# Performance work log

Measured on AMD Instinct MI355X. Metric: run time of the kernel, lower is better.

Reference implementation:

```python
import jax, jax.numpy as jnp
import numpy as np

H = 4  # attention heads
NEG = -1e9

def _ln(x, g, b):
    m = jnp.mean(x, -1, keepdims=True)
    v = jnp.var(x, -1, keepdims=True)
    return g * (x - m) * jax.lax.rsqrt(v + 1e-5) + b

def setup_inputs() -> dict:
    key = jax.random.key(0)
    ks = jax.random.split(key, 32)
    N, E, G, T = 4096, 128, 10, 10
    f32 = jnp.float32
    def w(k, shape, fan):
        return (jax.random.normal(k, shape, f32) / np.sqrt(fan)).astype(f32)
    inp = {
        'lora_states': jax.random.normal(ks[0], (N, 256), f32),
        'temperaments': jax.random.uniform(ks[1], (N, T), f32),
        'adjacency': jax.random.randint(ks[2], (N, N), 0, 2, jnp.int32),
        'memory_bank': jax.random.normal(ks[3], (G, E), f32) * 0.1,
        # lora_state_encoder: Linear(256,512) -> LN -> ReLU -> Linear(512,E) -> LN
        'enc_W1': w(ks[4], (256, 512), 256), 'enc_b1': jnp.zeros((512,), f32),
        'enc_g1': jnp.ones((512,), f32), 'enc_be1': jnp.zeros((512,), f32),
        'enc_W2': w(ks[5], (512, E), 512), 'enc_b2': jnp.zeros((E,), f32),
        'enc_g2': jnp.ones((E,), f32), 'enc_be2': jnp.zeros((E,), f32),
        # TemperamentEncoder: Linear(10,E) + tanh
        'temp_W': w(ks[6], (T, E), T), 'temp_b': jnp.zeros((E,), f32),
        # SocialAttentionLayer (adjacency-masked MHA)
        'Wq': w(ks[7], (E, E), E), 'Wk': w(ks[8], (E, E), E),
        'Wv': w(ks[9], (E, E), E), 'Wo': w(ks[10], (E, E), E),
        # PersonalityModulatedAttention scalar gate over [my_temp; ctx_j]
        'gate_wa': w(ks[11], (E,), E), 'gate_wb': w(ks[12], (E,), E),
        'gate_b': jnp.zeros((), f32),
        # lora_state_decoder: Linear(E,512) -> LN -> ReLU -> Linear(512,256)
        'dec_W1': w(ks[13], (E, 512), E), 'dec_b1': jnp.zeros((512,), f32),
        'dec_g1': jnp.ones((512,), f32), 'dec_be1': jnp.zeros((512,), f32),
        'dec_W2': w(ks[14], (512, 256), 512), 'dec_b2': jnp.zeros((256,), f32),
    }
    return inp

def reference(lora_states, temperaments, adjacency, memory_bank,
              enc_W1, enc_b1, enc_g1, enc_be1, enc_W2, enc_b2, enc_g2, enc_be2,
              temp_W, temp_b, Wq, Wk, Wv, Wo, gate_wa, gate_wb, gate_b,
              dec_W1, dec_b1, dec_g1, dec_be1, dec_W2, dec_b2):
    N = lora_states.shape[0]
    E = Wq.shape[0]
    dh = E // H
    # --- encode LoRA states ---
    h = jax.nn.relu(_ln(lora_states @ enc_W1 + enc_b1, enc_g1, enc_be1))
    emb = _ln(h @ enc_W2 + enc_b2, enc_g2, enc_be2)                  # [N,E]
    # --- temperament embeddings ---
    temp_emb = jnp.tanh(temperaments @ temp_W + temp_b)              # [N,E]
    # --- adjacency-masked multi-head social attention ---
    q = (emb @ Wq).reshape(N, H, dh).transpose(1, 0, 2)              # [H,N,dh]
    k = (emb @ Wk).reshape(N, H, dh).transpose(1, 0, 2)
    v = (emb @ Wv).reshape(N, H, dh).transpose(1, 0, 2)
    scores = jnp.einsum('hnd,hmd->hnm', q, k) / np.sqrt(dh)          # [H,N,N]
    adj = adjacency > 0
    eye = jnp.eye(N, dtype=bool)
    attn = jax.nn.softmax(jnp.where((adj | eye)[None], scores, NEG), axis=-1)
    ctx = jnp.einsum('hnm,hmd->hnd', attn, v).transpose(1, 0, 2).reshape(N, E) @ Wo  # [N,E]
    # --- personality-gated neighbor aggregation (scalar gate per (i,j)) ---
    ti = temp_emb @ gate_wa                                          # [N]
    cj = ctx @ gate_wb                                               # [N]
    gate = jax.nn.sigmoid(ti[:, None] + cj[None, :] + gate_b)        # [N,N]
    nmask = (adj & ~eye).astype(emb.dtype)                           # exclude self
    cnt = nmask.sum(-1)                                              # [N]
    combined = (nmask * gate) @ ctx / jnp.maximum(cnt, 1.0)[:, None] # mean of gated neighbor infos
    updated = emb + 0.2 * jnp.where(cnt[:, None] > 0, combined, 0.0)
    # --- generational memory retrieval: 0.9*emb + 0.1*ancestral ---
    mscore = updated @ memory_bank.T / np.sqrt(E)                    # [N,G]
    ancestral = jax.nn.softmax(mscore, axis=-1) @ memory_bank        # [N,E]
    updated = 0.9 * updated + 0.1 * ancestral
    # --- decode back to LoRA state vectors ---
    d = jax.nn.relu(_ln(updated @ dec_W1 + dec_b1, dec_g1, dec_be1))
    return d @ dec_W2 + dec_b2                                       # [N,256]
```

## Files before the change

kernel.cpp:

```cpp
#include <hip/hip_runtime.h>
#include <math.h>

#define N 4096
#define NHEAD 4
#define SPLIT_ATT 8
#define SPLIT_G 8

__global__ __launch_bounds__(256) void k_bm(const int* __restrict__ adj,
    unsigned int* __restrict__ bmw) {
  const int lane = threadIdx.x & 63;
  const int wid = threadIdx.x >> 6;
  const long total = (long)N * N / 64;
  long g = (long)blockIdx.x * 4 + wid;
  const long stride = (long)gridDim.x * 4;
  for (; g < total; g += stride) {
    int e = adj[g * 64 + lane];
    unsigned long long mask = __ballot(e != 0);
    if (lane == 0)  bmw[g * 2]     = (unsigned int)(mask & 0xFFFFFFFFull);
    if (lane == 32) bmw[g * 2 + 1] = (unsigned int)(mask >> 32);
  }
}

__global__ __launch_bounds__(512) void k_enc1(const float* __restrict__ X,
    const float* __restrict__ W, const float* __restrict__ b,
    const float* __restrict__ g, const float* __restrict__ be,
    float* __restrict__ out) {
  __shared__ float xs[8][256];
  __shared__ float hs[8][512];
  const int t = threadIdx.x;
  const int row0 = blockIdx.x * 8;
  {
    const float4* src = reinterpret_cast<const float4*>(X + row0 * 256);
    float4* dst = reinterpret_cast<float4*>(&xs[0][0]);
    dst[t] = src[t];
  }
  __syncthreads();
  float acc[8] = {0.f,0.f,0.f,0.f,0.f,0.f,0.f,0.f};
  for (int k = 0; k < 256; ++k) {
    float w = W[k * 512 + t];
#pragma unroll
    for (int r = 0; r < 8; ++r) acc[r] = fmaf(xs[r][k], w, acc[r]);
  }
  const float bb = b[t];
#pragma unroll
  for (int r = 0; r < 8; ++r) hs[r][t] = acc[r] + bb;
  __syncthreads();
  const int wv = t >> 6, lane = t & 63;
  float v0[8];
  float s1 = 0.f, s2 = 0.f;
#pragma unroll
  for (int kk = 0; kk < 8; ++kk) {
    float x = hs[wv][lane + 64 * kk];
    v0[kk] = x; s1 += x; s2 += x * x;
  }
#pragma unroll
  for (int off = 1; off < 64; off <<= 1) { s1 += __shfl_xor(s1, off); s2 += __shfl_xor(s2, off); }
  const float mean = s1 * (1.f / 512.f);
  const float var = s2 * (1.f / 512.f) - mean * mean;
  const float rstd = rsqrtf(var + 1e-5f);
#pragma unroll
  for (int kk = 0; kk < 8; ++kk) {
    int c = lane + 64 * kk;
    float y = g[c] * (v0[kk] - mean) * rstd + be[c];
    out[(row0 + wv) * 512 + c] = fmaxf(y, 0.f);
  }
}

__global__ __launch_bounds__(128) void k_enc2(const float* __restrict__ X,
    const float* __restrict__ W, const float* __restrict__ b,
    const float* __restrict__ g, const float* __restrict__ be,
    float* __restrict__ out) {
  __shared__ float xs[8][512];
  __shared__ float hs[8][128];
  const int t = threadIdx.x;
  const int row0 = blockIdx.x * 8;
  {
    const float4* src = reinterpret_cast<const float4*>(X + row0 * 512);
    float4* dst = reinterpret_cast<float4*>(&xs[0][0]);
    for (int idx = t; idx < 1024; idx += 128) dst[idx] = src[idx];
  }
  __syncthreads();
  float acc[8] = {0.f,0.f,0.f,0.f,0.f,0.f,0.f,0.f};
  for (int k = 0; k < 512; ++k) {
    float w = W[k * 128 + t];
#pragma unroll
    for (int r = 0; r < 8; ++r) acc[r] = fmaf(xs[r][k], w, acc[r]);
  }
  const float bb = b[t];
#pragma unroll
  for (int r = 0; r < 8; ++r) hs[r][t] = acc[r] + bb;
  __syncthreads();
  const int wv = t >> 6, lane = t & 63;
  for (int rr = 0; rr < 4; ++rr) {
    int row = wv * 4 + rr;
    float a0 = hs[row][lane], a1 = hs[row][lane + 64];
    float s1 = a0 + a1, s2 = a0 * a0 + a1 * a1;
#pragma unroll
    for (int off = 1; off < 64; off <<= 1) { s1 += __shfl_xor(s1, off); s2 += __shfl_xor(s2, off); }
    float mean = s1 * (1.f / 128.f);
    float rstd = rsqrtf(s2 * (1.f / 128.f) - mean * mean + 1e-5f);
    out[(row0 + row) * 128 + lane]      = g[lane] * (a0 - mean) * rstd + be[lane];
    out[(row0 + row) * 128 + lane + 64] = g[lane + 64] * (a1 - mean) * rstd + be[lane + 64];
  }
}

__global__ __launch_bounds__(512) void k_qkv(const float* __restrict__ emb,
    const float* __restrict__ Wq, const float* __restrict__ Wk, const float* __restrict__ Wv,
    float* __restrict__ q, float* __restrict__ k, float* __restrict__ v) {
  __shared__ float xs[16][128];
  const int t = threadIdx.x;
  const int col = t & 127;
  const int grp = t >> 7;
  const int row0 = blockIdx.x * 16;
  {
    const float4* src = reinterpret_cast<const float4*>(emb + row0 * 128);
    float4* dst = reinterpret_cast<float4*>(&xs[0][0]);
    dst[t] = src[t];
  }
  __syncthreads();
  float aq[4] = {0.f,0.f,0.f,0.f};
  float ak[4] = {0.f,0.f,0.f,0.f};
  float av[4] = {0.f,0.f,0.f,0.f};
  for (int kk = 0; kk < 128; ++kk) {
    float wq = Wq[kk * 128 + col], wk = Wk[kk * 128 + col], wv = Wv[kk * 128 + col];
#pragma unroll
    for (int r = 0; r < 4; ++r) {
      float x = xs[grp * 4 + r][kk];
      aq[r] = fmaf(x, wq, aq[r]);
      ak[r] = fmaf(x, wk, ak[r]);
      av[r] = fmaf(x, wv, av[r]);
    }
  }
#pragma unroll
  for (int r = 0; r < 4; ++r) {
    const int row = row0 + grp * 4 + r;
    q[row * 128 + col] = aq[r];
    k[row * 128 + col] = ak[r];
    v[row * 128 + col] = av[r];
  }
}

__global__ __launch_bounds__(256) void k_ti(const float* __restrict__ temps,
    const float* __restrict__ tW, const float* __restrict__ tb,
    const float* __restrict__ wa, float* __restrict__ ti_out) {
  __shared__ float tws[1280];
  __shared__ float tbs[128], was[128];
  const int t = threadIdx.x;
  for (int idx = t; idx < 1280; idx += 256) tws[idx] = tW[idx];
  if (t < 128) { tbs[t] = tb[t]; was[t] = wa[t]; }
  __syncthreads();
  const int qi = t & 3;
  const int li = t >> 2;
  const int i = blockIdx.x * 64 + li;
  float tp[10];
#pragma unroll
  for (int c = 0; c < 10; ++c) tp[c] = temps[i * 10 + c];
  float acc = 0.f;
  const int e0 = qi * 32;
  for (int e = e0; e < e0 + 32; ++e) {
    float s = tbs[e];
#pragma unroll
    for (int c = 0; c < 10; ++c) s = fmaf(tp[c], tws[c * 128 + e], s);
    float th = 1.f - 2.f * __fdividef(1.f, __expf(2.f * s) + 1.f);
    acc = fmaf(th, was[e], acc);
  }
  acc += __shfl_xor(acc, 1);
  acc += __shfl_xor(acc, 2);
  if (qi == 0) ti_out[i] = acc;
}

__global__ __launch_bounds__(256, 2) void k_attn(const float* __restrict__ q,
    const float* __restrict__ kk, const float* __restrict__ vv,
    const unsigned int* __restrict__ bmw,
    float* __restrict__ pacc, float* __restrict__ pml) {
  __shared__ float Kt[64][128];
  __shared__ float Vt[64][128];
  const int t = threadIdx.x;
  const int itile = blockIdx.x / SPLIT_ATT;
  const int split = blockIdx.x % SPLIT_ATT;
  const int h = t >> 6;
  const int row = t & 63;
  const int i = itile * 64 + row;
  const int dbase = h * 32;
  float4 q4[8];
  {
    const float4* qp = reinterpret_cast<const float4*>(q + (size_t)i * 128 + dbase);
#pragma unroll
    for (int u = 0; u < 8; ++u) q4[u] = qp[u];
  }
  float m = -1e30f, l = 0.f;
  float4 a[8];
#pragma unroll
  for (int u = 0; u < 8; ++u) a[u] = make_float4(0.f, 0.f, 0.f, 0.f);
  const int j0beg = split * (N / SPLIT_ATT);
  const int j0end = j0beg + (N / SPLIT_ATT);
  for (int j0 = j0beg; j0 < j0end; j0 += 64) {
    __syncthreads();
    {
      const float4* ks = reinterpret_cast<const float4*>(kk + (size_t)j0 * 128);
      const float4* vs = reinterpret_cast<const float4*>(vv + (size_t)j0 * 128);
      float4* kd = reinterpret_cast<float4*>(&Kt[0][0]);
      float4* vd = reinterpret_cast<float4*>(&Vt[0][0]);
#pragma unroll
      for (int u = 0; u < 8; ++u) { kd[t + 256 * u] = ks[t + 256 * u]; vd[t + 256 * u] = vs[t + 256 * u]; }
    }
    const uint2 mw = *reinterpret_cast<const uint2*>(bmw + (size_t)i * 128 + (j0 >> 5));
    const int eyeoff = i - j0;
    __syncthreads();
    for (int sub = 0; sub < 8; ++sub) {
      const int jb = sub * 8;
      unsigned mbits = ((sub < 4 ? mw.x : mw.y) >> ((sub & 3) * 8)) & 0xFFu;
      if (((unsigned)(eyeoff - jb)) < 8u) mbits |= (1u << (eyeoff - jb));
      float sarr[8];
#pragma unroll
      for (int u = 0; u < 8; ++u) {
        const float4* kp = reinterpret_cast<const float4*>(&Kt[jb + u][dbase]);
        float4 kf[8];
#pragma unroll
        for (int w = 0; w < 8; ++w) kf[w] = kp[w];
        float s0 = 0.f, s1 = 0.f, s2 = 0.f, s3 = 0.f;
#pragma unroll
        for (int w = 0; w < 8; ++w) {
          s0 = fmaf(q4[w].x, kf[w].x, s0);
          s1 = fmaf(q4[w].y, kf[w].y, s1);
          s2 = fmaf(q4[w].z, kf[w].z, s2);
          s3 = fmaf(q4[w].w, kf[w].w, s3);
        }
        sarr[u] = fmaf((s0 + s1) + (s2 + s3), 0.17677669529663687f,
                       ((mbits >> u) & 1u) ? 0.f : -1e9f);
      }
      float smax = fmaxf(fmaxf(fmaxf(sarr[0], sarr[1]), fmaxf(sarr[2], sarr[3])),
                         fmaxf(fmaxf(sarr[4], sarr[5]), fmaxf(sarr[6], sarr[7])));
      float mnew = fmaxf(m, smax);
      float r = __expf(m - mnew);
      m = mnew;
      l *= r;
#pragma unroll
      for (int u = 0; u < 8; ++u) {
        a[u].x *= r; a[u].y *= r; a[u].z *= r; a[u].w *= r;
      }
#pragma unroll
      for (int u = 0; u < 8; ++u) {
        float p = __expf(sarr[u] - m);
        l += p;
        const float4* vp = reinterpret_cast<const float4*>(&Vt[jb + u][dbase]);
#pragma unroll
        for (int w = 0; w < 8; ++w) {
          float4 vf = vp[w];
          a[w].x = fmaf(p, vf.x, a[w].x);
          a[w].y = fmaf(p, vf.y, a[w].y);
          a[w].z = fmaf(p, vf.z, a[w].z);
          a[w].w = fmaf(p, vf.w, a[w].w);
        }
      }
    }
  }
  {
    float4* pa4 = reinterpret_cast<float4*>(pacc + ((size_t)split * N + i) * 128 + dbase);
#pragma unroll
    for (int u = 0; u < 8; ++u) pa4[u] = a[u];
  }
  {
    float2* p2 = reinterpret_cast<float2*>(pml + (((size_t)split * N + i) * NHEAD + h) * 2);
    *p2 = make_float2(m, l);
  }
}

__global__ __launch_bounds__(256) void k_attn_comb(const float* __restrict__ pacc,
    const float* __restrict__ pml, float* __restrict__ attnout) {
  const int gid = blockIdx.x * 256 + threadIdx.x;
  const int i = gid >> 7, e = gid & 127, h = e >> 5;
  float ms[SPLIT_ATT], ls[SPLIT_ATT];
  float M = -1e30f;
#pragma unroll
  for (int s = 0; s < SPLIT_ATT; ++s) {
    size_t idx = (((size_t)s * N + i) * NHEAD + h) * 2;
    ms[s] = pml[idx]; ls[s] = pml[idx + 1];
    M = fmaxf(M, ms[s]);
  }
  float L = 0.f, o = 0.f;
#pragma unroll
  for (int s = 0; s < SPLIT_ATT; ++s) {
    float w = expf(ms[s] - M);
    L = fmaf(ls[s], w, L);
    o = fmaf(pacc[((size_t)(s * N + i)) * 128 + e], w, o);
  }
  attnout[gid] = o / L;
}

__global__ __launch_bounds__(128) void k_ctx(const float* __restrict__ att,
    const float* __restrict__ Wo, const float* __restrict__ wb,
    float* __restrict__ ctx, float* __restrict__ cj) {
  __shared__ float xs[8][128];
  __shared__ float hs[8][128];
  const int t = threadIdx.x;
  const int row0 = blockIdx.x * 8;
  {
    const float4* src = reinterpret_cast<const float4*>(att + row0 * 128);
    float4* dst = reinterpret_cast<float4*>(&xs[0][0]);
    for (int idx = t; idx < 256; idx += 128) dst[idx] = src[idx];
  }
  __syncthreads();
  float acc[8] = {0.f,0.f,0.f,0.f,0.f,0.f,0.f,0.f};
  for (int k = 0; k < 128; ++k) {
    float w = Wo[k * 128 + t];
#pragma unroll
    for (int r = 0; r < 8; ++r) acc[r] = fmaf(xs[r][k], w, acc[r]);
  }
  const float wbt = wb[t];
#pragma unroll
  for (int r = 0; r < 8; ++r) {
    ctx[(row0 + r) * 128 + t] = acc[r];
    hs[r][t] = acc[r] * wbt;
  }
  __syncthreads();
  const int wv = t >> 6, lane = t & 63;
  for (int rr = 0; rr < 4; ++rr) {
    int row = wv * 4 + rr;
    float s1 = hs[row][lane] + hs[row][lane + 64];
#pragma unroll
    for (int off = 1; off < 64; off <<= 1) s1 += __shfl_xor(s1, off);
    if (lane == 0) cj[row0 + row] = s1;
  }
}

__global__ __launch_bounds__(256) void k_gate(const float* __restrict__ ctx,
    const float* __restrict__ cj, const float* __restrict__ ti,
    const unsigned int* __restrict__ bmw, const float* __restrict__ gbp,
    float* __restrict__ pacc, float* __restrict__ pcnt) {
  __shared__ float cs[64][128];
  __shared__ float gtsT[64][65];
  __shared__ float tis[64];
  __shared__ float cntrow[64];
  __shared__ float pcsum[256];
  const int t = threadIdx.x;
  const int itile = blockIdx.x >> 3;
  const int split = blockIdx.x & 7;
  const int ig = t >> 4;
  const int eg = t & 15;
  const int i0 = itile * 64;
  const float gb = gbp[0];
  if (t < 64) { tis[t] = ti[i0 + t]; cntrow[t] = 0.f; }
  float acc[4][8];
#pragma unroll
  for (int r = 0; r < 4; ++r)
#pragma unroll
    for (int c = 0; c < 8; ++c) acc[r][c] = 0.f;
  const int j0beg = split * (N / SPLIT_G);
  const int j0end = j0beg + (N / SPLIT_G);
  for (int j0 = j0beg; j0 < j0end; j0 += 64) {
    __syncthreads();
    {
      const float4* src = reinterpret_cast<const float4*>(ctx + (size_t)j0 * 128);
      float4* dst = reinterpret_cast<float4*>(&cs[0][0]);
#pragma unroll
      for (int u = 0; u < 8; ++u) dst[t + 256 * u] = src[t + 256 * u];
    }
    {
      const int ii = t >> 2;
      const int qd = t & 3;
      const int jb = qd * 16;
      const int gi = i0 + ii;
      const float tii = tis[ii];
      const unsigned word = bmw[(size_t)gi * 128 + (j0 >> 5) + (qd >> 1)];
      const unsigned mb16 = (word >> ((qd & 1) * 16)) & 0xFFFFu;
      float cnt_loc = 0.f;
      const float4* cjp = reinterpret_cast<const float4*>(cj + j0 + jb);
      float4 cv[4];
#pragma unroll
      for (int u = 0; u < 4; ++u) cv[u] = cjp[u];
      const float cva[16] = {cv[0].x,cv[0].y,cv[0].z,cv[0].w, cv[1].x,cv[1].y,cv[1].z,cv[1].w,
                             cv[2].x,cv[2].y,cv[2].z,cv[2].w, cv[3].x,cv[3].y,cv[3].z,cv[3].w};
#pragma unroll
      for (int w = 0; w < 16; ++w) {
        const int gj = j0 + jb + w;
        const bool live = ((mb16 >> w) & 1u) && (gj != gi);
        float gval = 0.f;
        if (live) {
          gval = __fdividef(1.f, 1.f + __expf(-(tii + cva[w] + gb)));
          cnt_loc += 1.f;
        }
        gtsT[jb + w][ii] = gval;
      }
      pcsum[t] = cnt_loc;
    }
    __syncthreads();
    if (t < 64) {
      cntrow[t] += pcsum[t * 4] + pcsum[t * 4 + 1] + pcsum[t * 4 + 2] + pcsum[t * 4 + 3];
    }
    const int ib = ig * 4;
    const int eb = eg * 8;
    for (int jj = 0; jj < 64; ++jj) {
      const float a0 = gtsT[jj][ib + 0];
      const float a1 = gtsT[jj][ib + 1];
      const float a2 = gtsT[jj][ib + 2];
      const float a3 = gtsT[jj][ib + 3];
      const float4 b0 = *reinterpret_cast<const float4*>(&cs[jj][eb]);
      const float4 b1 = *reinterpret_cast<const float4*>(&cs[jj][eb + 4]);
      const float bv[8] = {b0.x, b0.y, b0.z, b0.w, b1.x, b1.y, b1.z, b1.w};
#pragma unroll
      for (int c = 0; c < 8; ++c) {
        acc[0][c] = fmaf(a0, bv[c], acc[0][c]);
        acc[1][c] = fmaf(a1, bv[c], acc[1][c]);
        acc[2][c] = fmaf(a2, bv[c], acc[2][c]);
        acc[3][c] = fmaf(a3, bv[c], acc[3][c]);
      }
    }
  }
#pragma unroll
  for (int r = 0; r < 4; ++r) {
    float* pa = pacc + ((size_t)split * N + i0 + ig * 4 + r) * 128 + eg * 8;
    float4 o0; o0.x = acc[r][0]; o0.y = acc[r][1]; o0.z = acc[r][2]; o0.w = acc[r][3];
    float4 o1; o1.x = acc[r][4]; o1.y = acc[r][5]; o1.z = acc[r][6]; o1.w = acc[r][7];
    reinterpret_cast<float4*>(pa)[0] = o0;
    reinterpret_cast<float4*>(pa)[1] = o1;
  }
  if (t < 64) pcnt[(size_t)split * N + i0 + t] = cntrow[t];
}

__global__ __launch_bounds__(256) void k_gcomb(const float* __restrict__ GA,
    const float* __restrict__ GC, const float* __restrict__ emb,
    const float* __restrict__ mb, float* __restrict__ upd) {
  __shared__ float mbs[10][128];
  __shared__ float us[2][128];
  const int t = threadIdx.x;
  for (int idx = t; idx < 1280; idx += 256) mbs[idx / 128][idx & 127] = mb[idx];
  const int rs = t >> 7, e = t & 127;
  const int i = blockIdx.x * 2 + rs;
  float a = 0.f;
#pragma unroll
  for (int s = 0; s < SPLIT_G; ++s) a += GA[((size_t)(s * N + i)) * 128 + e];
  float c = 0.f;
#pragma unroll
  for (int s = 0; s < SPLIT_G; ++s) c += GC[s * N + i];
  float comb = a / fmaxf(c, 1.f);
  float u = emb[(size_t)i * 128 + e] + 0.2f * ((c > 0.f) ? comb : 0.f);
  us[rs][e] = u;
  __syncthreads();
  const int wv = t >> 6, lane = t & 63;
  if (wv < 2) {
    const int i2 = blockIdx.x * 2 + wv;
    float u0 = us[wv][lane], u1 = us[wv][lane + 64];
    float sc[10];
#pragma unroll
    for (int g = 0; g < 10; ++g) {
      float p = u0 * mbs[g][lane] + u1 * mbs[g][lane + 64];
#pragma unroll
      for (int off = 1; off < 64; off <<= 1) p += __shfl_xor(p, off);
      sc[g] = p * 0.08838834764831845f;
    }
    float mx = sc[0];
#pragma unroll
    for (int g = 1; g < 10; ++g) mx = fmaxf(mx, sc[g]);
    float sum = 0.f;
#pragma unroll
    for (int g = 0; g < 10; ++g) { sc[g] = expf(sc[g] - mx); sum += sc[g]; }
    float inv = 1.f / sum;
    float anc0 = 0.f, anc1 = 0.f;
#pragma unroll
    for (int g = 0; g < 10; ++g) {
      float pg = sc[g] * inv;
      anc0 = fmaf(pg, mbs[g][lane], anc0);
      anc1 = fmaf(pg, mbs[g][lane + 64], anc1);
    }
    upd[(size_t)i2 * 128 + lane]      = 0.9f * u0 + 0.1f * anc0;
    upd[(size_t)i2 * 128 + lane + 64] = 0.9f * u1 + 0.1f * anc1;
  }
}

__global__ __launch_bounds__(512) void k_dec1(const float* __restrict__ X,
    const float* __restrict__ W, const float* __restrict__ b,
    const float* __restrict__ g, const float* __restrict__ be,
    float* __restrict__ out) {
  __shared__ float xs[8][128];
  __shared__ float hs[8][512];
  const int t = threadIdx.x;
  const int row0 = blockIdx.x * 8;
  if (t < 256) {
    const float4* src = reinterpret_cast<const float4*>(X + row0 * 128);
    float4* dst = reinterpret_cast<float4*>(&xs[0][0]);
    dst[t] = src[t];
  }
  __syncthreads();
  float acc[8] = {0.f,0.f,0.f,0.f,0.f,0.f,0.f,0.f};
  for (int k = 0; k < 128; ++k) {
    float w = W[k * 512 + t];
#pragma unroll
    for (int r = 0; r < 8; ++r) acc[r] = fmaf(xs[r][k], w, acc[r]);
  }
  const float bb = b[t];
#pragma unroll
  for (int r = 0; r < 8; ++r) hs[r][t] = acc[r] + bb;
  __syncthreads();
  const int wv = t >> 6, lane = t & 63;
  float v0[8];
  float s1 = 0.f, s2 = 0.f;
#pragma unroll
  for (int kk = 0; kk < 8; ++kk) {
    float x = hs[wv][lane + 64 * kk];
    v0[kk] = x; s1 += x; s2 += x * x;
  }
#pragma unroll
  for (int off = 1; off < 64; off <<= 1) { s1 += __shfl_xor(s1, off); s2 += __shfl_xor(s2, off); }
  const float mean = s1 * (1.f / 512.f);
  const float var = s2 * (1.f / 512.f) - mean * mean;
  const float rstd = rsqrtf(var + 1e-5f);
#pragma unroll
  for (int kk = 0; kk < 8; ++kk) {
    int c = lane + 64 * kk;
    float y = g[c] * (v0[kk] - mean) * rstd + be[c];
    out[(row0 + wv) * 512 + c] = fmaxf(y, 0.f);
  }
}

__global__ __launch_bounds__(256) void k_dec2(const float* __restrict__ X,
    const float* __restrict__ W, const float* __restrict__ b, float* __restrict__ out) {
  __shared__ float xs[8][512];
  const int t = threadIdx.x;
  const int row0 = blockIdx.x * 8;
  {
    const float4* src = reinterpret_cast<const float4*>(X + row0 * 512);
    float4* dst = reinterpret_cast<float4*>(&xs[0][0]);
    for (int idx = t; idx < 1024; idx += 256) dst[idx] = src[idx];
  }
  __syncthreads();
  float acc[8] = {0.f,0.f,0.f,0.f,0.f,0.f,0.f,0.f};
  for (int k = 0; k < 512; ++k) {
    float w = W[k * 256 + t];
#pragma unroll
    for (int r = 0; r < 8; ++r) acc[r] = fmaf(xs[r][k], w, acc[r]);
  }
  const float bb = b[t];
#pragma unroll
  for (int r = 0; r < 8; ++r) out[(row0 + r) * 256 + t] = acc[r] + bb;
}

extern "C" void kernel_launch(void* const* d_in, const int* in_sizes, int n_in,
                              void* d_out, int out_size, void* d_ws, size_t ws_size,
                              hipStream_t stream) {
  const float* lora   = (const float*)d_in[0];
  const float* temps  = (const float*)d_in[1];
  const int*   adj    = (const int*)d_in[2];
  const float* mb     = (const float*)d_in[3];
  const float* enc_W1 = (const float*)d_in[4];
  const float* enc_b1 = (const float*)d_in[5];
  const float* enc_g1 = (const float*)d_in[6];
  const float* enc_be1= (const float*)d_in[7];
  const float* enc_W2 = (const float*)d_in[8];
  const float* enc_b2 = (const float*)d_in[9];
  const float* enc_g2 = (const float*)d_in[10];
  const float* enc_be2= (const float*)d_in[11];
  const float* temp_W = (const float*)d_in[12];
  const float* temp_b = (const float*)d_in[13];
  const float* Wq     = (const float*)d_in[14];
  const float* Wk     = (const float*)d_in[15];
  const float* Wv     = (const float*)d_in[16];
  const float* Wo     = (const float*)d_in[17];
  const float* g_wa   = (const float*)d_in[18];
  const float* g_wb   = (const float*)d_in[19];
  const float* g_b    = (const float*)d_in[20];
  const float* dec_W1 = (const float*)d_in[21];
  const float* dec_b1 = (const float*)d_in[22];
  const float* dec_g1 = (const float*)d_in[23];
  const float* dec_be1= (const float*)d_in[24];
  const float* dec_W2 = (const float*)d_in[25];
  const float* dec_b2 = (const float*)d_in[26];

  float* ws = (float*)d_ws;
  float* H1  = ws;
  float* EMB = H1 + (size_t)N * 512;
  float* Q   = EMB + (size_t)N * 128;
  float* K   = Q + (size_t)N * 128;
  float* V   = K + (size_t)N * 128;
  float* ATT = V + (size_t)N * 128;
  float* CTX = ATT + (size_t)N * 128;
  float* TI  = CTX + (size_t)N * 128;
  float* CJ  = TI + N;
  float* PA  = CJ + N;
  float* PML = PA + (size_t)8 * N * 128;
  unsigned int* BMW = (unsigned int*)(PML + (size_t)8 * N * NHEAD * 2);
  float* UPD = ATT;
  float* GA  = PA;
  float* GC  = PML;
  float* DEC = H1;

  k_bm<<<512, 256, 0, stream>>>(adj, BMW);
  k_enc1<<<N / 8, 512, 0, stream>>>(lora, enc_W1, enc_b1, enc_g1, enc_be1, H1);
  k_enc2<<<N / 8, 128, 0, stream>>>(H1, enc_W2, enc_b2, enc_g2, enc_be2, EMB);
  k_ti<<<N / 64, 256, 0, stream>>>(temps, temp_W, temp_b, g_wa, TI);
  k_qkv<<<N / 16, 512, 0, stream>>>(EMB, Wq, Wk, Wv, Q, K, V);
  k_attn<<<(N / 64) * SPLIT_ATT, 256, 0, stream>>>(Q, K, V, BMW, PA, PML);
  k_attn_comb<<<(N * 128) / 256, 256, 0, stream>>>(PA, PML, ATT);
  k_ctx<<<N / 8, 128, 0, stream>>>(ATT, Wo, g_wb, CTX, CJ);
  k_gate<<<(N / 64) * SPLIT_G, 256, 0, stream>>>(CTX, CJ, TI, BMW, g_b, GA, GC);
  k_gcomb<<<N / 2, 256, 0, stream>>>(GA, GC, EMB, mb, UPD);
  k_dec1<<<N / 8, 512, 0, stream>>>(UPD, dec_W1, dec_b1, dec_g1, dec_be1, DEC);
  k_dec2<<<N / 8, 256, 0, stream>>>(DEC, dec_W2, dec_b2, (float*)d_out);
}
```

Baseline: 716.7 us.

## Retune attention split and tiles, vectorize LDS reads in dense GEMM kernels

```diff
diff --git a/kernel.cpp b/kernel.cpp
--- a/kernel.cpp
+++ b/kernel.cpp
@@ -3,7 +3,7 @@
 
 #define N 4096
 #define NHEAD 4
-#define SPLIT_ATT 8
+#define SPLIT_ATT 16
 #define SPLIT_G 8
 
 __global__ __launch_bounds__(256) void k_bm(const int* __restrict__ adj,
@@ -21,7 +21,7 @@
   }
 }
 
-__global__ __launch_bounds__(512) void k_enc1(const float* __restrict__ X,
+__global__ __launch_bounds__(256) void k_enc1(const float* __restrict__ X,
     const float* __restrict__ W, const float* __restrict__ b,
     const float* __restrict__ g, const float* __restrict__ be,
     float* __restrict__ out) {
@@ -32,41 +32,57 @@
   {
     const float4* src = reinterpret_cast<const float4*>(X + row0 * 256);
     float4* dst = reinterpret_cast<float4*>(&xs[0][0]);
-    dst[t] = src[t];
-  }
-  __syncthreads();
-  float acc[8] = {0.f,0.f,0.f,0.f,0.f,0.f,0.f,0.f};
-  for (int k = 0; k < 256; ++k) {
-    float w = W[k * 512 + t];
-#pragma unroll
-    for (int r = 0; r < 8; ++r) acc[r] = fmaf(xs[r][k], w, acc[r]);
-  }
-  const float bb = b[t];
-#pragma unroll
-  for (int r = 0; r < 8; ++r) hs[r][t] = acc[r] + bb;
+    dst[t] = src[t]; dst[t + 256] = src[t + 256];
+  }
+  __syncthreads();
+  float acc0[8], acc1[8];
+#pragma unroll
+  for (int r = 0; r < 8; ++r) { acc0[r] = 0.f; acc1[r] = 0.f; }
+  for (int k4 = 0; k4 < 64; ++k4) {
+    const int k = k4 * 4;
+    const float w00 = W[(k + 0) * 512 + t];
+    const float w01 = W[(k + 1) * 512 + t];
+    const float w02 = W[(k + 2) * 512 + t];
+    const float w03 = W[(k + 3) * 512 + t];
+    const float w10 = W[(k + 0) * 512 + t + 256];
+    const float w11 = W[(k + 1) * 512 + t + 256];
+    const float w12 = W[(k + 2) * 512 + t + 256];
+    const float w13 = W[(k + 3) * 512 + t + 256];
+#pragma unroll
+    for (int r = 0; r < 8; ++r) {
+      const float4 xv = *reinterpret_cast<const float4*>(&xs[r][k]);
+      acc0[r] = fmaf(xv.x, w00, fmaf(xv.y, w01, fmaf(xv.z, w02, fmaf(xv.w, w03, acc0[r]))));
+      acc1[r] = fmaf(xv.x, w10, fmaf(xv.y, w11, fmaf(xv.z, w12, fmaf(xv.w, w13, acc1[r]))));
+    }
+  }
+  const float b0 = b[t], b1 = b[t + 256];
+#pragma unroll
+  for (int r = 0; r < 8; ++r) { hs[r][t] = acc0[r] + b0; hs[r][t + 256] = acc1[r] + b1; }
   __syncthreads();
   const int wv = t >> 6, lane = t & 63;
-  float v0[8];
-  float s1 = 0.f, s2 = 0.f;
-#pragma unroll
-  for (int kk = 0; kk < 8; ++kk) {
-    float x = hs[wv][lane + 64 * kk];
-    v0[kk] = x; s1 += x; s2 += x * x;
-  }
-#pragma unroll
-  for (int off = 1; off < 64; off <<= 1) { s1 += __shfl_xor(s1, off); s2 += __shfl_xor(s2, off); }
-  const float mean = s1 * (1.f / 512.f);
-  const float var = s2 * (1.f / 512.f) - mean * mean;
-  const float rstd = rsqrtf(var + 1e-5f);
-#pragma unroll
-  for (int kk = 0; kk < 8; ++kk) {
-    int c = lane + 64 * kk;
-    float y = g[c] * (v0[kk] - mean) * rstd + be[c];
-    out[(row0 + wv) * 512 + c] = fmaxf(y, 0.f);
-  }
-}
-
-__global__ __launch_bounds__(128) void k_enc2(const float* __restrict__ X,
+  for (int rr = 0; rr < 2; ++rr) {
+    const int row = wv * 2 + rr;
+    float v0[8];
+    float s1 = 0.f, s2 = 0.f;
+#pragma unroll
+    for (int kk = 0; kk < 8; ++kk) {
+      float x = hs[row][lane + 64 * kk];
+      v0[kk] = x; s1 += x; s2 += x * x;
+    }
+#pragma unroll
+    for (int off = 1; off < 64; off <<= 1) { s1 += __shfl_xor(s1, off); s2 += __shfl_xor(s2, off); }
+    const float mean = s1 * (1.f / 512.f);
+    const float rstd = rsqrtf(s2 * (1.f / 512.f) - mean * mean + 1e-5f);
+#pragma unroll
+    for (int kk = 0; kk < 8; ++kk) {
+      int c = lane + 64 * kk;
+      float y = g[c] * (v0[kk] - mean) * rstd + be[c];
+      out[(row0 + row) * 512 + c] = fmaxf(y, 0.f);
+    }
+  }
+}
+
+__global__ __launch_bounds__(256) void k_enc2(const float* __restrict__ X,
     const float* __restrict__ W, const float* __restrict__ b,
     const float* __restrict__ g, const float* __restrict__ be,
     float* __restrict__ out) {
@@ -77,22 +93,32 @@
   {
     const float4* src = reinterpret_cast<const float4*>(X + row0 * 512);
     float4* dst = reinterpret_cast<float4*>(&xs[0][0]);
-    for (int idx = t; idx < 1024; idx += 128) dst[idx] = src[idx];
-  }
-  __syncthreads();
-  float acc[8] = {0.f,0.f,0.f,0.f,0.f,0.f,0.f,0.f};
-  for (int k = 0; k < 512; ++k) {
-    float w = W[k * 128 + t];
-#pragma unroll
-    for (int r = 0; r < 8; ++r) acc[r] = fmaf(xs[r][k], w, acc[r]);
-  }
-  const float bb = b[t];
-#pragma unroll
-  for (int r = 0; r < 8; ++r) hs[r][t] = acc[r] + bb;
+#pragma unroll
+    for (int u = 0; u < 4; ++u) dst[t + 256 * u] = src[t + 256 * u];
+  }
+  __syncthreads();
+  const int col = t & 127;
+  const int rg = t >> 7;
+  float acc[4] = {0.f,0.f,0.f,0.f};
+  for (int k4 = 0; k4 < 128; ++k4) {
+    const int k = k4 * 4;
+    const float w0 = W[(k + 0) * 128 + col];
+    const float w1 = W[(k + 1) * 128 + col];
+    const float w2 = W[(k + 2) * 128 + col];
+    const float w3 = W[(k + 3) * 128 + col];
+#pragma unroll
+    for (int r = 0; r < 4; ++r) {
+      const float4 xv = *reinterpret_cast<const float4*>(&xs[rg * 4 + r][k]);
+      acc[r] = fmaf(xv.x, w0, fmaf(xv.y, w1, fmaf(xv.z, w2, fmaf(xv.w, w3, acc[r]))));
+    }
+  }
+  const float bb = b[col];
+#pragma unroll
+  for (int r = 0; r < 4; ++r) hs[rg * 4 + r][col] = acc[r] + bb;
   __syncthreads();
   const int wv = t >> 6, lane = t & 63;
-  for (int rr = 0; rr < 4; ++rr) {
-    int row = wv * 4 + rr;
+  for (int rr = 0; rr < 2; ++rr) {
+    const int row = wv * 2 + rr;
     float a0 = hs[row][lane], a1 = hs[row][lane + 64];
     float s1 = a0 + a1, s2 = a0 * a0 + a1 * a1;
 #pragma unroll
@@ -121,14 +147,17 @@
   float aq[4] = {0.f,0.f,0.f,0.f};
   float ak[4] = {0.f,0.f,0.f,0.f};
   float av[4] = {0.f,0.f,0.f,0.f};
-  for (int kk = 0; kk < 128; ++kk) {
-    float wq = Wq[kk * 128 + col], wk = Wk[kk * 128 + col], wv = Wv[kk * 128 + col];
+  for (int k4 = 0; k4 < 32; ++k4) {
+    const int kk = k4 * 4;
+    float wq0 = Wq[(kk+0)*128+col], wq1 = Wq[(kk+1)*128+col], wq2 = Wq[(kk+2)*128+col], wq3 = Wq[(kk+3)*128+col];
+    float wk0 = Wk[(kk+0)*128+col], wk1 = Wk[(kk+1)*128+col], wk2 = Wk[(kk+2)*128+col], wk3 = Wk[(kk+3)*128+col];
+    float wv0 = Wv[(kk+0)*128+col], wv1 = Wv[(kk+1)*128+col], wv2 = Wv[(kk+2)*128+col], wv3 = Wv[(kk+3)*128+col];
 #pragma unroll
     for (int r = 0; r < 4; ++r) {
-      float x = xs[grp * 4 + r][kk];
-      aq[r] = fmaf(x, wq, aq[r]);
-      ak[r] = fmaf(x, wk, ak[r]);
-      av[r] = fmaf(x, wv, av[r]);
+      const float4 xv = *reinterpret_cast<const float4*>(&xs[grp * 4 + r][kk]);
+      aq[r] = fmaf(xv.x, wq0, fmaf(xv.y, wq1, fmaf(xv.z, wq2, fmaf(xv.w, wq3, aq[r]))));
+      ak[r] = fmaf(xv.x, wk0, fmaf(xv.y, wk1, fmaf(xv.z, wk2, fmaf(xv.w, wk3, ak[r]))));
+      av[r] = fmaf(xv.x, wv0, fmaf(xv.y, wv1, fmaf(xv.z, wv2, fmaf(xv.w, wv3, av[r]))));
     }
   }
 #pragma unroll
@@ -169,12 +198,12 @@
   if (qi == 0) ti_out[i] = acc;
 }
 
-__global__ __launch_bounds__(256, 2) void k_attn(const float* __restrict__ q,
+__global__ __launch_bounds__(256, 4) void k_attn(const float* __restrict__ q,
     const float* __restrict__ kk, const float* __restrict__ vv,
     const unsigned int* __restrict__ bmw,
     float* __restrict__ pacc, float* __restrict__ pml) {
-  __shared__ float Kt[64][128];
-  __shared__ float Vt[64][128];
+  __shared__ float Kt[32][128];
+  __shared__ float Vt[32][128];
   const int t = threadIdx.x;
   const int itile = blockIdx.x / SPLIT_ATT;
   const int split = blockIdx.x % SPLIT_ATT;
@@ -192,9 +221,10 @@
   float4 a[8];
 #pragma unroll
   for (int u = 0; u < 8; ++u) a[u] = make_float4(0.f, 0.f, 0.f, 0.f);
-  const int j0beg = split * (N / SPLIT_ATT);
-  const int j0end = j0beg + (N / SPLIT_ATT);
-  for (int j0 = j0beg; j0 < j0end; j0 += 64) {
+  const int jrange = N / SPLIT_ATT;
+  const int j0beg = split * jrange;
+  const int j0end = j0beg + jrange;
+  for (int j0 = j0beg; j0 < j0end; j0 += 32) {
     __syncthreads();
     {
       const float4* ks = reinterpret_cast<const float4*>(kk + (size_t)j0 * 128);
@@ -202,14 +232,14 @@
       float4* kd = reinterpret_cast<float4*>(&Kt[0][0]);
       float4* vd = reinterpret_cast<float4*>(&Vt[0][0]);
 #pragma unroll
-      for (int u = 0; u < 8; ++u) { kd[t + 256 * u] = ks[t + 256 * u]; vd[t + 256 * u] = vs[t + 256 * u]; }
-    }
-    const uint2 mw = *reinterpret_cast<const uint2*>(bmw + (size_t)i * 128 + (j0 >> 5));
+      for (int u = 0; u < 4; ++u) { kd[t + 256 * u] = ks[t + 256 * u]; vd[t + 256 * u] = vs[t + 256 * u]; }
+    }
+    const unsigned mword = bmw[(size_t)i * 128 + (j0 >> 5)];
     const int eyeoff = i - j0;
     __syncthreads();
-    for (int sub = 0; sub < 8; ++sub) {
+    for (int sub = 0; sub < 4; ++sub) {
       const int jb = sub * 8;
-      unsigned mbits = ((sub < 4 ? mw.x : mw.y) >> ((sub & 3) * 8)) & 0xFFu;
+      unsigned mbits = (mword >> jb) & 0xFFu;
       if (((unsigned)(eyeoff - jb)) < 8u) mbits |= (1u << (eyeoff - jb));
       float sarr[8];
 #pragma unroll
@@ -217,27 +247,29 @@
         const float4* kp = reinterpret_cast<const float4*>(&Kt[jb + u][dbase]);
         float4 kf[8];
 #pragma unroll
-        for (int w = 0; w < 8; ++w) kf[w] = kp[w];
+        for (int x = 0; x < 8; ++x) kf[x] = kp[x];
         float s0 = 0.f, s1 = 0.f, s2 = 0.f, s3 = 0.f;
 #pragma unroll
-        for (int w = 0; w < 8; ++w) {
-          s0 = fmaf(q4[w].x, kf[w].x, s0);
-          s1 = fmaf(q4[w].y, kf[w].y, s1);
-          s2 = fmaf(q4[w].z, kf[w].z, s2);
-          s3 = fmaf(q4[w].w, kf[w].w, s3);
+        for (int x = 0; x < 8; ++x) {
+          s0 = fmaf(q4[x].x, kf[x].x, s0);
+          s1 = fmaf(q4[x].y, kf[x].y, s1);
+          s2 = fmaf(q4[x].z, kf[x].z, s2);
+          s3 = fmaf(q4[x].w, kf[x].w, s3);
         }
         sarr[u] = fmaf((s0 + s1) + (s2 + s3), 0.17677669529663687f,
                        ((mbits >> u) & 1u) ? 0.f : -1e9f);
       }
       float smax = fmaxf(fmaxf(fmaxf(sarr[0], sarr[1]), fmaxf(sarr[2], sarr[3])),
                          fmaxf(fmaxf(sarr[4], sarr[5]), fmaxf(sarr[6], sarr[7])));
-      float mnew = fmaxf(m, smax);
-      float r = __expf(m - mnew);
-      m = mnew;
-      l *= r;
-#pragma unroll
-      for (int u = 0; u < 8; ++u) {
-        a[u].x *= r; a[u].y *= r; a[u].z *= r; a[u].w *= r;
+      if (__any(smax > m)) {
+        float mnew = fmaxf(m, smax);
+        float r = __expf(m - mnew);
+        m = mnew;
+        l *= r;
+#pragma unroll
+        for (int u = 0; u < 8; ++u) {
+          a[u].x *= r; a[u].y *= r; a[u].z *= r; a[u].w *= r;
+        }
       }
 #pragma unroll
       for (int u = 0; u < 8; ++u) {
@@ -245,12 +277,12 @@
         l += p;
         const float4* vp = reinterpret_cast<const float4*>(&Vt[jb + u][dbase]);
 #pragma unroll
-        for (int w = 0; w < 8; ++w) {
-          float4 vf = vp[w];
-          a[w].x = fmaf(p, vf.x, a[w].x);
-          a[w].y = fmaf(p, vf.y, a[w].y);
-          a[w].z = fmaf(p, vf.z, a[w].z);
-          a[w].w = fmaf(p, vf.w, a[w].w);
+        for (int x = 0; x < 8; ++x) {
+          float4 vf = vp[x];
+          a[x].x = fmaf(p, vf.x, a[x].x);
+          a[x].y = fmaf(p, vf.y, a[x].y);
+          a[x].z = fmaf(p, vf.z, a[x].z);
+          a[x].w = fmaf(p, vf.w, a[x].w);
         }
       }
     }
@@ -288,36 +320,45 @@
   attnout[gid] = o / L;
 }
 
-__global__ __launch_bounds__(128) void k_ctx(const float* __restrict__ att,
+__global__ __launch_bounds__(512) void k_ctx(const float* __restrict__ att,
     const float* __restrict__ Wo, const float* __restrict__ wb,
     float* __restrict__ ctx, float* __restrict__ cj) {
-  __shared__ float xs[8][128];
-  __shared__ float hs[8][128];
-  const int t = threadIdx.x;
-  const int row0 = blockIdx.x * 8;
+  __shared__ float xs[16][128];
+  __shared__ float hs[16][128];
+  const int t = threadIdx.x;
+  const int row0 = blockIdx.x * 16;
   {
     const float4* src = reinterpret_cast<const float4*>(att + row0 * 128);
     float4* dst = reinterpret_cast<float4*>(&xs[0][0]);
-    for (int idx = t; idx < 256; idx += 128) dst[idx] = src[idx];
-  }
-  __syncthreads();
-  float acc[8] = {0.f,0.f,0.f,0.f,0.f,0.f,0.f,0.f};
-  for (int k = 0; k < 128; ++k) {
-    float w = Wo[k * 128 + t];
-#pragma unroll
-    for (int r = 0; r < 8; ++r) acc[r] = fmaf(xs[r][k], w, acc[r]);
-  }
-  const float wbt = wb[t];
-#pragma unroll
-  for (int r = 0; r < 8; ++r) {
-    ctx[(row0 + r) * 128 + t] = acc[r];
-    hs[r][t] = acc[r] * wbt;
+    dst[t] = src[t];
+  }
+  __syncthreads();
+  const int col = t & 127;
+  const int grp = t >> 7;
+  float acc[4] = {0.f,0.f,0.f,0.f};
+  for (int k4 = 0; k4 < 32; ++k4) {
+    const int k = k4 * 4;
+    const float w0 = Wo[(k + 0) * 128 + col];
+    const float w1 = Wo[(k + 1) * 128 + col];
+    const float w2 = Wo[(k + 2) * 128 + col];
+    const float w3 = Wo[(k + 3) * 128 + col];
+#pragma unroll
+    for (int r = 0; r < 4; ++r) {
+      const float4 xv = *reinterpret_cast<const float4*>(&xs[grp * 4 + r][k]);
+      acc[r] = fmaf(xv.x, w0, fmaf(xv.y, w1, fmaf(xv.z, w2, fmaf(xv.w, w3, acc[r]))));
+    }
+  }
+#pragma unroll
+  for (int r = 0; r < 4; ++r) {
+    ctx[(row0 + grp * 4 + r) * 128 + col] = acc[r];
+    hs[grp * 4 + r][col] = acc[r];
   }
   __syncthreads();
   const int wv = t >> 6, lane = t & 63;
-  for (int rr = 0; rr < 4; ++rr) {
-    int row = wv * 4 + rr;
-    float s1 = hs[row][lane] + hs[row][lane + 64];
+  const float wb0 = wb[lane], wb1 = wb[lane + 64];
+  for (int rr = 0; rr < 2; ++rr) {
+    const int row = wv * 2 + rr;
+    float s1 = hs[row][lane] * wb0 + hs[row][lane + 64] * wb1;
 #pragma unroll
     for (int off = 1; off < 64; off <<= 1) s1 += __shfl_xor(s1, off);
     if (lane == 0) cj[row0 + row] = s1;
@@ -468,7 +509,7 @@
   }
 }
 
-__global__ __launch_bounds__(512) void k_dec1(const float* __restrict__ X,
+__global__ __launch_bounds__(256) void k_dec1(const float* __restrict__ X,
     const float* __restrict__ W, const float* __restrict__ b,
     const float* __restrict__ g, const float* __restrict__ be,
     float* __restrict__ out) {
@@ -476,40 +517,56 @@
   __shared__ float hs[8][512];
   const int t = threadIdx.x;
   const int row0 = blockIdx.x * 8;
-  if (t < 256) {
+  {
     const float4* src = reinterpret_cast<const float4*>(X + row0 * 128);
     float4* dst = reinterpret_cast<float4*>(&xs[0][0]);
     dst[t] = src[t];
   }
   __syncthreads();
-  float acc[8] = {0.f,0.f,0.f,0.f,0.f,0.f,0.f,0.f};
-  for (int k = 0; k < 128; ++k) {
-    float w = W[k * 512 + t];
-#pragma unroll
-    for (int r = 0; r < 8; ++r) acc[r] = fmaf(xs[r][k], w, acc[r]);
-  }
-  const float bb = b[t];
-#pragma unroll
-  for (int r = 0; r < 8; ++r) hs[r][t] = acc[r] + bb;
+  float acc0[8], acc1[8];
+#pragma unroll
+  for (int r = 0; r < 8; ++r) { acc0[r] = 0.f; acc1[r] = 0.f; }
+  for (int k4 = 0; k4 < 32; ++k4) {
+    const int k = k4 * 4;
+    const float w00 = W[(k + 0) * 512 + t];
+    const float w01 = W[(k + 1) * 512 + t];
+    const float w02 = W[(k + 2) * 512 + t];
+    const float w03 = W[(k + 3) * 512 + t];
+    const float w10 = W[(k + 0) * 512 + t + 256];
+    const float w11 = W[(k + 1) * 512 + t + 256];
+    const float w12 = W[(k + 2) * 512 + t + 256];
+    const float w13 = W[(k + 3) * 512 + t + 256];
+#pragma unroll
+    for (int r = 0; r < 8; ++r) {
+      const float4 xv = *reinterpret_cast<const float4*>(&xs[r][k]);
+      acc0[r] = fmaf(xv.x, w00, fmaf(xv.y, w01, fmaf(xv.z, w02, fmaf(xv.w, w03, acc0[r]))));
+      acc1[r] = fmaf(xv.x, w10, fmaf(xv.y, w11, fmaf(xv.z, w12, fmaf(xv.w, w13, acc1[r]))));
+    }
+  }
+  const float b0 = b[t], b1 = b[t + 256];
+#pragma unroll
+  for (int r = 0; r < 8; ++r) { hs[r][t] = acc0[r] + b0; hs[r][t + 256] = acc1[r] + b1; }
   __syncthreads();
   const int wv = t >> 6, lane = t & 63;
-  float v0[8];
-  float s1 = 0.f, s2 = 0.f;
-#pragma unroll
-  for (int kk = 0; kk < 8; ++kk) {
-    float x = hs[wv][lane + 64 * kk];
-    v0[kk] = x; s1 += x; s2 += x * x;
-  }
-#pragma unroll
-  for (int off = 1; off < 64; off <<= 1) { s1 += __shfl_xor(s1, off); s2 += __shfl_xor(s2, off); }
-  const float mean = s1 * (1.f / 512.f);
-  const float var = s2 * (1.f / 512.f) - mean * mean;
-  const float rstd = rsqrtf(var + 1e-5f);
-#pragma unroll
-  for (int kk = 0; kk < 8; ++kk) {
-    int c = lane + 64 * kk;
-    float y = g[c] * (v0[kk] - mean) * rstd + be[c];
-    out[(row0 + wv) * 512 + c] = fmaxf(y, 0.f);
+  for (int rr = 0; rr < 2; ++rr) {
+    const int row = wv * 2 + rr;
+    float v0[8];
+    float s1 = 0.f, s2 = 0.f;
+#pragma unroll
+    for (int kk = 0; kk < 8; ++kk) {
+      float x = hs[row][lane + 64 * kk];
+      v0[kk] = x; s1 += x; s2 += x * x;
+    }
+#pragma unroll
+    for (int off = 1; off < 64; off <<= 1) { s1 += __shfl_xor(s1, off); s2 += __shfl_xor(s2, off); }
+    const float mean = s1 * (1.f / 512.f);
+    const float rstd = rsqrtf(s2 * (1.f / 512.f) - mean * mean + 1e-5f);
+#pragma unroll
+    for (int kk = 0; kk < 8; ++kk) {
+      int c = lane + 64 * kk;
+      float y = g[c] * (v0[kk] - mean) * rstd + be[c];
+      out[(row0 + row) * 512 + c] = fmaxf(y, 0.f);
+    }
   }
 }
 
@@ -521,14 +578,24 @@
   {
     const float4* src = reinterpret_cast<const float4*>(X + row0 * 512);
     float4* dst = reinterpret_cast<float4*>(&xs[0][0]);
-    for (int idx = t; idx < 1024; idx += 256) dst[idx] = src[idx];
-  }
-  __syncthreads();
-  float acc[8] = {0.f,0.f,0.f,0.f,0.f,0.f,0.f,0.f};
-  for (int k = 0; k < 512; ++k) {
-    float w = W[k * 256 + t];
-#pragma unroll
-    for (int r = 0; r < 8; ++r) acc[r] = fmaf(xs[r][k], w, acc[r]);
+#pragma unroll
+    for (int u = 0; u < 4; ++u) dst[t + 256 * u] = src[t + 256 * u];
+  }
+  __syncthreads();
+  float acc[8];
+#pragma unroll
+  for (int r = 0; r < 8; ++r) acc[r] = 0.f;
+  for (int k4 = 0; k4 < 128; ++k4) {
+    const int k = k4 * 4;
+    const float w0 = W[(k + 0) * 256 + t];
+    const float w1 = W[(k + 1) * 256 + t];
+    const float w2 = W[(k + 2) * 256 + t];
+    const float w3 = W[(k + 3) * 256 + t];
+#pragma unroll
+    for (int r = 0; r < 8; ++r) {
+      const float4 xv = *reinterpret_cast<const float4*>(&xs[r][k]);
+      acc[r] = fmaf(xv.x, w0, fmaf(xv.y, w1, fmaf(xv.z, w2, fmaf(xv.w, w3, acc[r]))));
+    }
   }
   const float bb = b[t];
 #pragma unroll
@@ -577,23 +644,23 @@
   float* TI  = CTX + (size_t)N * 128;
   float* CJ  = TI + N;
   float* PA  = CJ + N;
-  float* PML = PA + (size_t)8 * N * 128;
-  unsigned int* BMW = (unsigned int*)(PML + (size_t)8 * N * NHEAD * 2);
+  float* PML = PA + (size_t)SPLIT_ATT * N * 128;
+  unsigned int* BMW = (unsigned int*)(PML + (size_t)SPLIT_ATT * N * NHEAD * 2);
   float* UPD = ATT;
   float* GA  = PA;
   float* GC  = PML;
   float* DEC = H1;
 
   k_bm<<<512, 256, 0, stream>>>(adj, BMW);
-  k_enc1<<<N / 8, 512, 0, stream>>>(lora, enc_W1, enc_b1, enc_g1, enc_be1, H1);
-  k_enc2<<<N / 8, 128, 0, stream>>>(H1, enc_W2, enc_b2, enc_g2, enc_be2, EMB);
+  k_enc1<<<N / 8, 256, 0, stream>>>(lora, enc_W1, enc_b1, enc_g1, enc_be1, H1);
+  k_enc2<<<N / 8, 256, 0, stream>>>(H1, enc_W2, enc_b2, enc_g2, enc_be2, EMB);
   k_ti<<<N / 64, 256, 0, stream>>>(temps, temp_W, temp_b, g_wa, TI);
   k_qkv<<<N / 16, 512, 0, stream>>>(EMB, Wq, Wk, Wv, Q, K, V);
   k_attn<<<(N / 64) * SPLIT_ATT, 256, 0, stream>>>(Q, K, V, BMW, PA, PML);
   k_attn_comb<<<(N * 128) / 256, 256, 0, stream>>>(PA, PML, ATT);
-  k_ctx<<<N / 8, 128, 0, stream>>>(ATT, Wo, g_wb, CTX, CJ);
+  k_ctx<<<N / 16, 512, 0, stream>>>(ATT, Wo, g_wb, CTX, CJ);
   k_gate<<<(N / 64) * SPLIT_G, 256, 0, stream>>>(CTX, CJ, TI, BMW, g_b, GA, GC);
   k_gcomb<<<N / 2, 256, 0, stream>>>(GA, GC, EMB, mb, UPD);
-  k_dec1<<<N / 8, 512, 0, stream>>>(UPD, dec_W1, dec_b1, dec_g1, dec_be1, DEC);
+  k_dec1<<<N / 8, 256, 0, stream>>>(UPD, dec_W1, dec_b1, dec_g1, dec_be1, DEC);
   k_dec2<<<N / 8, 256, 0, stream>>>(DEC, dec_W2, dec_b2, (float*)d_out);
 }
```

Measured after the change: 625.7 us. 1.15x faster.
